# Performance work log

Hardware: AMD Instinct MI355X
Metric: run time of the kernel (lower is better)

## Reference

```python
import jax, jax.numpy as jnp
import numpy as np

HEADS = 16
D_MODEL = 1024
D_K = D_MODEL // HEADS


def setup_inputs() -> dict:
    key = jax.random.key(0)
    ks = jax.random.split(key, 12)
    B, S = 4, 2048
    scale = 1.0 / np.sqrt(D_MODEL)
    inp = {
        'q': jax.random.normal(ks[0], (B, S, D_MODEL), jnp.float32),
        'k': jax.random.normal(ks[1], (B, S, D_MODEL), jnp.float32),
        'v': jax.random.normal(ks[2], (B, S, D_MODEL), jnp.float32),
        'Wq': jax.random.normal(ks[3], (D_MODEL, D_MODEL), jnp.float32) * scale,
        'bq': jnp.zeros((D_MODEL,), jnp.float32),
        'Wk': jax.random.normal(ks[4], (D_MODEL, D_MODEL), jnp.float32) * scale,
        'bk': jnp.zeros((D_MODEL,), jnp.float32),
        'Wv': jax.random.normal(ks[5], (D_MODEL, D_MODEL), jnp.float32) * scale,
        'bv': jnp.zeros((D_MODEL,), jnp.float32),
        'Wo': jax.random.normal(ks[6], (D_MODEL, D_MODEL), jnp.float32) * scale,
        'bo': jnp.zeros((D_MODEL,), jnp.float32),
    }
    return inp


def reference(q, k, v, Wq, bq, Wk, bk, Wv, bv, Wo, bo):
    B, S, _ = q.shape
    # linear projections, split into heads: [B, H, S, Dk]
    def proj(x, W, b):
        return (x @ W.T + b).reshape(B, -1, HEADS, D_K).transpose(0, 2, 1, 3)
    qh = proj(q, Wq, bq)
    kh = proj(k, Wk, bk)
    vh = proj(v, Wv, bv)
    scores = jnp.einsum('bhsd,bhtd->bhst', qh, kh) / jnp.sqrt(jnp.float32(D_K))
    attn = jax.nn.softmax(scores, axis=-1)
    ctx = jnp.einsum('bhst,bhtd->bhsd', attn, vh)  # [B,H,S,Dk]
    concat = ctx.transpose(0, 2, 1, 3).reshape(B, S, D_MODEL)
    return concat @ Wo.T + bo
```

## Files before the change

### kernel.cpp

```cpp
#include <hip/hip_runtime.h>
#include <hip/hip_bf16.h>


typedef __attribute__((ext_vector_type(8))) short short8;
typedef __attribute__((ext_vector_type(4))) float f32x4;
typedef __attribute__((ext_vector_type(16))) float f32x16;

#define DEV __device__ __forceinline__

DEV ushort f2bf(float f) {
  union { float f; unsigned u; } v; v.f = f;
  return (ushort)((v.u + 0x7fffu + ((v.u >> 16) & 1u)) >> 16);
}

DEV void gload_lds16(const void* g, void* lds) {
  __builtin_amdgcn_global_load_lds(
      (const __attribute__((address_space(1))) void*)g,
      (__attribute__((address_space(3))) void*)lds, 16, 0, 0);
}

__global__ void cvt_kernel(const float* __restrict__ in, ushort* __restrict__ out, int n4) {
  int stride = gridDim.x * blockDim.x;
  for (int i = blockIdx.x * blockDim.x + threadIdx.x; i < n4; i += stride) {
    float4 v = ((const float4*)in)[i];
    ushort4 o;
    o.x = f2bf(v.x); o.y = f2bf(v.y); o.z = f2bf(v.z); o.w = f2bf(v.w);
    ((ushort4*)out)[i] = o;
  }
}

__global__ void cvtw_kernel(const float* __restrict__ a, const float* __restrict__ b,
                            const float* __restrict__ c, const float* __restrict__ d,
                            ushort* __restrict__ oa, ushort* __restrict__ ob,
                            ushort* __restrict__ oc, ushort* __restrict__ od, int n4) {
  const float* s[4] = {a, b, c, d};
  ushort* o[4] = {oa, ob, oc, od};
  const float* src = s[blockIdx.y];
  ushort* dst = o[blockIdx.y];
  int stride = gridDim.x * blockDim.x;
  for (int i = blockIdx.x * blockDim.x + threadIdx.x; i < n4; i += stride) {
    float4 v = ((const float4*)src)[i];
    ushort4 u;
    u.x = f2bf(v.x); u.y = f2bf(v.y); u.z = f2bf(v.z); u.w = f2bf(v.w);
    ((ushort4*)dst)[i] = u;
  }
}

template<int MODE>
__global__ __launch_bounds__(256) void gemm_bt(
    const ushort* __restrict__ X, const ushort* __restrict__ W,
    const float* __restrict__ bias, void* __restrict__ out)
{
  constexpr int K = 1024, N = 1024;
  __shared__ __align__(16) ushort As[128 * 64];
  __shared__ __align__(16) ushort Bs[128 * 64];
  const int t = threadIdx.x;
  const int w = t >> 6, l = t & 63;
  const int bid = blockIdx.x;
  const int m0 = (bid >> 3) * 128, n0 = (bid & 7) * 128;
  const int wm = (w >> 1) * 64, wn = (w & 1) * 64;

  const f32x4 zero = {0.f, 0.f, 0.f, 0.f};
  f32x4 acc[4][4];
#pragma unroll
  for (int i = 0; i < 4; i++)
#pragma unroll
    for (int j = 0; j < 4; j++) acc[i][j] = zero;

  const int srow = t >> 3;
  const int scol = ((t & 7) ^ (srow & 7)) << 4;
  const char* xg = (const char*)X + (size_t)(m0 + srow) * 2048 + scol;
  const char* wg = (const char*)W + (size_t)(n0 + srow) * 2048 + scol;
  char* asl = (char*)As + t * 16;
  char* bsl = (char*)Bs + t * 16;

  const int swf = (l & 7) << 4;

  for (int kt = 0; kt < K; kt += 64) {
    __syncthreads();
#pragma unroll
    for (int pass = 0; pass < 4; pass++) {
      gload_lds16(xg + (size_t)pass * 32 * 2048 + kt * 2, asl + pass * 4096);
      gload_lds16(wg + (size_t)pass * 32 * 2048 + kt * 2, bsl + pass * 4096);
    }
    __syncthreads();

#pragma unroll
    for (int h = 0; h < 2; h++) {
      short8 af[4], bf[4];
#pragma unroll
      for (int i = 0; i < 4; i++) {
        int ra = wm + i * 16 + (l & 15);
        int rb = wn + i * 16 + (l & 15);
        int cb = (h * 64 + (l >> 4) * 16) ^ swf;
        af[i] = *(const short8*)((const char*)As + ra * 128 + cb);
        bf[i] = *(const short8*)((const char*)Bs + rb * 128 + cb);
      }
#pragma unroll
      for (int i = 0; i < 4; i++)
#pragma unroll
        for (int j = 0; j < 4; j++)
          acc[i][j] = __builtin_amdgcn_mfma_f32_16x16x32_bf16(af[i], bf[j], acc[i][j], 0, 0, 0);
    }
  }

#pragma unroll
  for (int i = 0; i < 4; i++) {
    int mbase = m0 + wm + i * 16 + ((l >> 4) << 2);
#pragma unroll
    for (int j = 0; j < 4; j++) {
      int n = n0 + wn + j * 16 + (l & 15);
      float bv = bias[n];
#pragma unroll
      for (int r = 0; r < 4; r++) {
        int m = mbase + r;
        float v = acc[i][j][r] + bv;
        if (MODE == 2) {
          ((float*)out)[(size_t)m * N + n] = v;
        } else {
          int b = m >> 11, s = m & 2047;
          int h = n >> 6, d = n & 63;
          size_t off;
          if (MODE == 0) off = ((size_t)(b * 16 + h) * 2048 + s) * 64 + d;
          else           off = ((size_t)(b * 16 + h) * 64 + d) * 2048 + s;
          ((ushort*)out)[off] = f2bf(v);
        }
      }
    }
  }
}

__global__ __launch_bounds__(256, 4) void attn_kernel(
    const ushort* __restrict__ Qh, const ushort* __restrict__ Kh,
    const ushort* __restrict__ Vt, ushort* __restrict__ ctx)
{
  __shared__ __align__(16) ushort Ks[2 * 64 * 64];
  __shared__ __align__(16) ushort Vs[2 * 64 * 64];
  const int t = threadIdx.x, w = t >> 6, l = t & 63;
  const int hf = l >> 5, ln = l & 31;
  const int p = blockIdx.x;
  const int logical = (p & 7) * 128 + (p >> 3);
  const int bh = logical >> 4;
  const int q0 = (logical & 15) * 128 + w * 32;
  const ushort* Qb = Qh + (size_t)bh * 2048 * 64;
  const ushort* Kb = Kh + (size_t)bh * 2048 * 64;
  const ushort* Vb = Vt + (size_t)bh * 64 * 2048;

  short8 qb[4];
  {
    const ushort* qp = Qb + (size_t)(q0 + ln) * 64 + hf * 8;
    const float SC = 0.18033688f;
#pragma unroll
    for (int s = 0; s < 4; s++) {
      short8 v = *(const short8*)(qp + s * 16);
#pragma unroll
      for (int j = 0; j < 8; j++) {
        union { float f; unsigned u; } x;
        x.u = ((unsigned)(ushort)v[j]) << 16;
        x.f *= SC;
        v[j] = (short)f2bf(x.f);
      }
      qb[s] = v;
    }
  }

  short8 ones;
#pragma unroll
  for (int j = 0; j < 8; j++) ones[j] = (short)0x3F80;

  f32x16 o_acc[2], o_l;
  f32x16 z16;
#pragma unroll
  for (int r = 0; r < 16; r++) z16[r] = 0.f;
  o_acc[0] = z16; o_acc[1] = z16; o_l = z16;

  const int srow = t >> 3;
  const int ssw = (((t & 7) ^ (srow & 7)) << 4);
  const char* kg = (const char*)Kb + (size_t)srow * 128 + ssw;
  const char* vg = (const char*)Vb + (size_t)srow * 4096 + ssw;
  char* kld = (char*)Ks + (size_t)t * 16;
  char* vld = (char*)Vs + (size_t)t * 16;

#define STAGE(buf_, kv0_) do {                                                  \
    gload_lds16(kg + (size_t)(kv0_) * 128, kld + (buf_) * 8192);                \
    gload_lds16(kg + (size_t)(kv0_) * 128 + 32 * 128, kld + (buf_) * 8192 + 4096); \
    gload_lds16(vg + (size_t)(kv0_) * 2, vld + (buf_) * 8192);                  \
    gload_lds16(vg + (size_t)(kv0_) * 2 + (size_t)32 * 4096, vld + (buf_) * 8192 + 4096); \
  } while (0)

  STAGE(0, 0);
  __syncthreads();

  const int rsw = (ln & 7) << 4;

  for (int it = 0; it < 32; it++) {
    const int cur = it & 1;
    if (it < 31) STAGE(cur ^ 1, (it + 1) * 64);
    const char* KsB = (const char*)Ks + cur * 8192;
    const char* VsB = (const char*)Vs + cur * 8192;

    f32x16 sf[2];
    __builtin_amdgcn_s_setprio(1);
#pragma unroll
    for (int f = 0; f < 2; f++) {
      f32x16 s_ = z16;
#pragma unroll
      for (int s = 0; s < 4; s++) {
        short8 kf = *(const short8*)(KsB + (32 * f + ln) * 128 + ((16 * hf + 32 * s) ^ rsw));
        s_ = __builtin_amdgcn_mfma_f32_32x32x16_bf16(kf, qb[s], s_, 0, 0, 0);
      }
      sf[f] = s_;
    }
    __builtin_amdgcn_s_setprio(0);

#pragma unroll
    for (int f = 0; f < 2; f++)
#pragma unroll
      for (int r = 0; r < 16; r++) sf[f][r] = __builtin_amdgcn_exp2f(sf[f][r]);

    __builtin_amdgcn_s_setprio(1);
#pragma unroll
    for (int f = 0; f < 2; f++) {
      unsigned wd0, wd1, wd2, wd3, wd4, wd5, wd6, wd7;
      asm("v_cvt_pk_bf16_f32 %0, %1, %2" : "=v"(wd0) : "v"(sf[f][0]),  "v"(sf[f][1]));
      asm("v_cvt_pk_bf16_f32 %0, %1, %2" : "=v"(wd1) : "v"(sf[f][2]),  "v"(sf[f][3]));
      asm("v_cvt_pk_bf16_f32 %0, %1, %2" : "=v"(wd2) : "v"(sf[f][4]),  "v"(sf[f][5]));
      asm("v_cvt_pk_bf16_f32 %0, %1, %2" : "=v"(wd3) : "v"(sf[f][6]),  "v"(sf[f][7]));
      asm("v_cvt_pk_bf16_f32 %0, %1, %2" : "=v"(wd4) : "v"(sf[f][8]),  "v"(sf[f][9]));
      asm("v_cvt_pk_bf16_f32 %0, %1, %2" : "=v"(wd5) : "v"(sf[f][10]), "v"(sf[f][11]));
      asm("v_cvt_pk_bf16_f32 %0, %1, %2" : "=v"(wd6) : "v"(sf[f][12]), "v"(sf[f][13]));
      asm("v_cvt_pk_bf16_f32 %0, %1, %2" : "=v"(wd7) : "v"(sf[f][14]), "v"(sf[f][15]));
      asm("v_permlane32_swap_b32 %0, %1" : "+v"(wd0), "+v"(wd2));
      asm("v_permlane32_swap_b32 %0, %1" : "+v"(wd1), "+v"(wd3));
      asm("v_permlane32_swap_b32 %0, %1" : "+v"(wd4), "+v"(wd6));
      asm("v_permlane32_swap_b32 %0, %1" : "+v"(wd5), "+v"(wd7));
#pragma unroll
      for (int s2 = 0; s2 < 2; s2++) {
        union { unsigned u[4]; short8 s8; } pa;
        if (s2 == 0) { pa.u[0] = wd0; pa.u[1] = wd1; pa.u[2] = wd2; pa.u[3] = wd3; }
        else         { pa.u[0] = wd4; pa.u[1] = wd5; pa.u[2] = wd6; pa.u[3] = wd7; }
        const int s = 2 * f + s2;
#pragma unroll
        for (int dn = 0; dn < 2; dn++) {
          short8 vf = *(const short8*)(VsB + (32 * dn + ln) * 128 + ((16 * hf + 32 * s) ^ rsw));
          o_acc[dn] = __builtin_amdgcn_mfma_f32_32x32x16_bf16(pa.s8, vf, o_acc[dn], 0, 0, 0);
        }
        o_l = __builtin_amdgcn_mfma_f32_32x32x16_bf16(pa.s8, ones, o_l, 0, 0, 0);
      }
    }
    __builtin_amdgcn_s_setprio(0);

    __syncthreads();
  }
#undef STAGE

  const int b = bh >> 4, hd = bh & 15;
#pragma unroll
  for (int r = 0; r < 16; r++) {
    int qrow = (r & 3) + 8 * (r >> 2) + 4 * hf;
    float inv = 1.f / o_l[r];
#pragma unroll
    for (int dn = 0; dn < 2; dn++) {
      int d = dn * 32 + ln;
      size_t off = (((size_t)b * 2048 + (q0 + qrow)) * 16 + hd) * 64 + d;
      ctx[off] = f2bf(o_acc[dn][r] * inv);
    }
  }
}

extern "C" void kernel_launch(void* const* d_in, const int* in_sizes, int n_in,
                              void* d_out, int out_size, void* d_ws, size_t ws_size,
                              hipStream_t stream) {
  const float* q  = (const float*)d_in[0];
  const float* k  = (const float*)d_in[1];
  const float* v  = (const float*)d_in[2];
  const float* Wq = (const float*)d_in[3];
  const float* bq = (const float*)d_in[4];
  const float* Wk = (const float*)d_in[5];
  const float* bk = (const float*)d_in[6];
  const float* Wv = (const float*)d_in[7];
  const float* bv = (const float*)d_in[8];
  const float* Wo = (const float*)d_in[9];
  const float* bo = (const float*)d_in[10];

  const size_t MSZ = (size_t)8192 * 1024;
  const size_t WSZ = (size_t)1024 * 1024;
  char* ws = (char*)d_ws;
  ushort* Xbuf = (ushort*)ws;
  ushort* w16[4];
  w16[0] = Xbuf + MSZ;
  w16[1] = w16[0] + WSZ;
  w16[2] = w16[1] + WSZ;
  w16[3] = w16[2] + WSZ;
  ushort* Qhb = w16[3] + WSZ;
  ushort* Khb = Qhb + MSZ;
  ushort* Vtb = Khb + MSZ;
  ushort* ctx = Xbuf;

  cvtw_kernel<<<dim3(256, 4), 256, 0, stream>>>(Wq, Wk, Wv, Wo,
                                                w16[0], w16[1], w16[2], w16[3],
                                                (int)(WSZ / 4));

  cvt_kernel<<<2048, 256, 0, stream>>>(q, Xbuf, (int)(MSZ / 4));
  gemm_bt<0><<<512, 256, 0, stream>>>(Xbuf, w16[0], bq, Qhb);
  cvt_kernel<<<2048, 256, 0, stream>>>(k, Xbuf, (int)(MSZ / 4));
  gemm_bt<0><<<512, 256, 0, stream>>>(Xbuf, w16[1], bk, Khb);
  cvt_kernel<<<2048, 256, 0, stream>>>(v, Xbuf, (int)(MSZ / 4));
  gemm_bt<1><<<512, 256, 0, stream>>>(Xbuf, w16[2], bv, Vtb);

  attn_kernel<<<dim3(1024), 256, 0, stream>>>(Qhb, Khb, Vtb, ctx);

  gemm_bt<2><<<512, 256, 0, stream>>>(ctx, w16[3], bo, (float*)d_out);
}
```

Baseline: 217.7 us.

## Double-buffer LDS tiles in projection GEMM to overlap loads with MFMA

The projection GEMM now uses two LDS buffers for the A and B tiles. It issues the global-to-LDS loads for the next k-step before computing on the current one, and drops one of the two barriers per iteration. The aim is to hide global load latency behind the MFMA work. This doubles LDS use to 64KB per block, which may lower occupancy. The loop also relies on one barrier per step, which must cover both load completion and the reuse of the old buffer.

```diff
diff --git a/kernel.cpp b/kernel.cpp
--- a/kernel.cpp
+++ b/kernel.cpp
@@ -52,8 +52,8 @@
     const float* __restrict__ bias, void* __restrict__ out)
 {
   constexpr int K = 1024, N = 1024;
-  __shared__ __align__(16) ushort As[128 * 64];
-  __shared__ __align__(16) ushort Bs[128 * 64];
+  __shared__ __align__(16) ushort As[2 * 128 * 64];
+  __shared__ __align__(16) ushort Bs[2 * 128 * 64];
   const int t = threadIdx.x;
   const int w = t >> 6, l = t & 63;
   const int bid = blockIdx.x;
@@ -74,16 +74,26 @@
   char* asl = (char*)As + t * 16;
   char* bsl = (char*)Bs + t * 16;
 
+#define GSTAGE(buf_, kt_) do {                                                   \
+    _Pragma("unroll")                                                            \
+    for (int pass = 0; pass < 4; pass++) {                                       \
+      gload_lds16(xg + (size_t)pass * 32 * 2048 + (kt_) * 2,                     \
+                  asl + (buf_) * 16384 + pass * 4096);                           \
+      gload_lds16(wg + (size_t)pass * 32 * 2048 + (kt_) * 2,                     \
+                  bsl + (buf_) * 16384 + pass * 4096);                           \
+    }                                                                            \
+  } while (0)
+
   const int swf = (l & 7) << 4;
 
-  for (int kt = 0; kt < K; kt += 64) {
-    __syncthreads();
-#pragma unroll
-    for (int pass = 0; pass < 4; pass++) {
-      gload_lds16(xg + (size_t)pass * 32 * 2048 + kt * 2, asl + pass * 4096);
-      gload_lds16(wg + (size_t)pass * 32 * 2048 + kt * 2, bsl + pass * 4096);
-    }
-    __syncthreads();
+  GSTAGE(0, 0);
+  __syncthreads();
+
+  for (int step = 0; step < 16; step++) {
+    const int cur = step & 1;
+    if (step < 15) GSTAGE(cur ^ 1, (step + 1) * 64);
+    const char* AsB = (const char*)As + cur * 16384;
+    const char* BsB = (const char*)Bs + cur * 16384;
 
 #pragma unroll
     for (int h = 0; h < 2; h++) {
@@ -93,8 +103,8 @@
         int ra = wm + i * 16 + (l & 15);
         int rb = wn + i * 16 + (l & 15);
         int cb = (h * 64 + (l >> 4) * 16) ^ swf;
-        af[i] = *(const short8*)((const char*)As + ra * 128 + cb);
-        bf[i] = *(const short8*)((const char*)Bs + rb * 128 + cb);
+        af[i] = *(const short8*)(AsB + ra * 128 + cb);
+        bf[i] = *(const short8*)(BsB + rb * 128 + cb);
       }
 #pragma unroll
       for (int i = 0; i < 4; i++)
@@ -102,7 +112,10 @@
         for (int j = 0; j < 4; j++)
           acc[i][j] = __builtin_amdgcn_mfma_f32_16x16x32_bf16(af[i], bf[j], acc[i][j], 0, 0, 0);
     }
-  }
+
+    __syncthreads();
+  }
+#undef GSTAGE
 
 #pragma unroll
   for (int i = 0; i < 4; i++) {
```

Measured after the change: 238.5 us. 9.5% more time.
